# Kernel tuning notes

Measured on AMD Instinct MI355X. Metric: run time of the kernel, lower is better.

Reference implementation:

```python
import jax, jax.numpy as jnp
import numpy as np

POS_TH = 0.5
NEG_TH = 0.4
NEGPOS_RATIO = 3
BBOX_ALPHA = 1.5
CONF_ALPHA = 1.0
VAR_CXCY = 0.1
VAR_WH = 0.2
NUM_CLASSES = 41
B, P, G = 8, 100000, 16


def setup_inputs() -> dict:
    key = jax.random.key(0)
    k = jax.random.split(key, 8)
    loc_data = jax.random.normal(k[0], (B, P, 4), dtype=jnp.float32)
    conf_data = jax.random.normal(k[1], (B, P, NUM_CLASSES), dtype=jnp.float32)
    # priors in (cx, cy, w, h), normalized coords
    p_cxy = jax.random.uniform(k[2], (P, 2), minval=0.0, maxval=1.0)
    p_wh = jax.random.uniform(k[3], (P, 2), minval=0.02, maxval=0.3)
    priors = jnp.concatenate([p_cxy, p_wh], axis=1).astype(jnp.float32)
    # gt boxes in point form (x1, y1, x2, y2)
    g_cxy = jax.random.uniform(k[4], (B, G, 2), minval=0.15, maxval=0.85)
    g_wh = jax.random.uniform(k[5], (B, G, 2), minval=0.05, maxval=0.4)
    gt_boxes = jnp.concatenate([
        jnp.clip(g_cxy - g_wh / 2, 0.0, 1.0),
        jnp.clip(g_cxy + g_wh / 2, 0.0, 1.0),
    ], axis=-1).astype(jnp.float32)
    gt_labels = jax.random.randint(k[6], (B, G), 1, NUM_CLASSES)
    return {"loc_data": loc_data, "conf_data": conf_data, "priors": priors,
            "gt_boxes": gt_boxes, "gt_labels": gt_labels}


def point_form(pr):
    return jnp.concatenate([pr[:, :2] - pr[:, 2:] / 2,
                            pr[:, :2] + pr[:, 2:] / 2], axis=1)


def jaccard(a, b):
    # a: [G,4] xyxy, b: [P,4] xyxy -> [G,P]
    lt = jnp.maximum(a[:, None, :2], b[None, :, :2])
    rb = jnp.minimum(a[:, None, 2:], b[None, :, 2:])
    wh = jnp.clip(rb - lt, 0.0)
    inter = wh[..., 0] * wh[..., 1]
    area_a = ((a[:, 2] - a[:, 0]) * (a[:, 3] - a[:, 1]))[:, None]
    area_b = ((b[:, 2] - b[:, 0]) * (b[:, 3] - b[:, 1]))[None, :]
    return inter / (area_a + area_b - inter)


def encode(matched, priors):
    # matched [P,4] xyxy, priors [P,4] cxcywh -> SSD offsets with variances
    g_cxcy = ((matched[:, :2] + matched[:, 2:]) / 2 - priors[:, :2]) / (VAR_CXCY * priors[:, 2:])
    g_wh = jnp.log(jnp.clip((matched[:, 2:] - matched[:, :2]) / priors[:, 2:], 1e-8)) / VAR_WH
    return jnp.concatenate([g_cxcy, g_wh], axis=1)


def match_one(gt_box, gt_label, priors):
    # gt_box [G,4], gt_label [G], priors [P,4] -> loc_t [P,4], conf_t [P]
    pf = point_form(priors)
    ov = jaccard(gt_box, pf)                      # [G,P]
    best_truth_ov = ov.max(axis=0)                # [P]
    best_truth_idx = ov.argmax(axis=0)            # [P]
    best_prior_idx = ov.argmax(axis=1)            # [G] best prior per gt
    # force-match each gt to its best prior
    best_truth_ov = best_truth_ov.at[best_prior_idx].set(2.0)
    best_truth_idx = best_truth_idx.at[best_prior_idx].set(jnp.arange(gt_box.shape[0]))
    conf = gt_label[best_truth_idx]
    conf = jnp.where(best_truth_ov < POS_TH, -1, conf)   # neutral
    conf = jnp.where(best_truth_ov < NEG_TH, 0, conf)    # background
    loc = encode(gt_box[best_truth_idx], priors)
    return loc, conf


def reference(loc_data, conf_data, priors, gt_boxes, gt_labels):
    bsz, n_pri, n_cls = conf_data.shape
    loc_t, conf_t = jax.vmap(match_one, in_axes=(0, 0, None))(gt_boxes, gt_labels, priors)
    pos = conf_t > 0                               # [B,P]
    num_pos = pos.sum(axis=1)                      # [B]
    # pos_weights: uniform 1/num_pos per image (ones split then normalized)
    pos_w = pos.astype(loc_data.dtype) / jnp.clip(num_pos, 1).astype(loc_data.dtype)[:, None]
    # localization: weighted SmoothL1 over positives
    d = loc_data - loc_t
    sl1 = jnp.where(jnp.abs(d) < 1.0, 0.5 * d * d, jnp.abs(d) - 0.5)
    loss_B = (pos_w[..., None] * sl1).sum() * BBOX_ALPHA
    # OHEM hard negative mining on background-suppression loss
    loss_c = jax.nn.logsumexp(conf_data, axis=-1) - conf_data[..., 0]
    loss_c = jnp.where(pos | (conf_t < 0), 0.0, loss_c)
    order = jnp.argsort(-loss_c, axis=1)
    rank = jnp.argsort(order, axis=1)
    num_neg = jnp.clip(NEGPOS_RATIO * num_pos, 0, n_pri - 1)
    neg = (rank < num_neg[:, None]) & (~pos) & (conf_t >= 0)
    keep = (pos | neg).astype(conf_data.dtype)
    logp = jax.nn.log_softmax(conf_data, axis=-1)
    ce = -jnp.take_along_axis(logp, jnp.clip(conf_t, 0)[..., None], axis=-1)[..., 0]
    total_pos = jnp.clip(num_pos.sum(), 1).astype(conf_data.dtype)
    loss_C = (ce * keep).sum() * CONF_ALPHA / total_pos
    return (loss_B + loss_C) / bsz
```

## Files before the change

kernel.cpp:

```cpp
#include <hip/hip_runtime.h>
#include <stdint.h>

#define BATCH 8
#define NPRI 100000
#define NGT 16
#define NCLS 41
#define F_POS_TH 0.5f
#define F_NEG_TH 0.4f

static constexpr int WTPB = 64;
static constexpr int CPT = WTPB * NCLS / 4;
static constexpr int BLK_PER_B = 224;
static constexpr int TILES_PER_B = (NPRI + WTPB - 1) / WTPB;
static constexpr int H0BIN = 256;
static constexpr int NBIN = 4096;

static constexpr size_t OFF_KEY  = 0;
static constexpr size_t OFF_GTC  = OFF_KEY + (size_t)BATCH*NPRI*4;
static constexpr size_t OFF_HG   = OFF_GTC + BATCH*NGT*8;
static constexpr size_t OFF_NPOS = OFF_HG + (size_t)BATCH*H0BIN*4;
static constexpr size_t OFF_SL1  = OFF_NPOS + BATCH*4;
static constexpr size_t OFF_CEP  = OFF_SL1  + BATCH*4;
static constexpr size_t OFF_NEG  = OFF_CEP  + BATCH*4;
static constexpr size_t OFF_FTK  = OFF_NEG  + BATCH*4;
static constexpr int ZERO_U32 = (int)((OFF_FTK + 4 - OFF_HG) / 4);

typedef float f32x4 __attribute__((ext_vector_type(4)));

__device__ inline float smoothl1(float d) {
  float a = fabsf(d);
  return a < 1.f ? 0.5f * d * d : a - 0.5f;
}
__device__ inline float sl1_terms(f32x4 pv, f32x4 ld, f32x4 gv) {
  float tx = ((gv[0] + gv[2]) * 0.5f - pv[0]) / (0.1f * pv[2]);
  float ty = ((gv[1] + gv[3]) * 0.5f - pv[1]) / (0.1f * pv[3]);
  float tw = __logf(fmaxf((gv[2] - gv[0]) / pv[2], 1e-8f)) / 0.2f;
  float th = __logf(fmaxf((gv[3] - gv[1]) / pv[3], 1e-8f)) / 0.2f;
  return smoothl1(ld[0] - tx) + smoothl1(ld[1] - ty)
       + smoothl1(ld[2] - tw) + smoothl1(ld[3] - th);
}
__device__ inline float aload_f32(const float* p) {
  return __hip_atomic_load(p, __ATOMIC_RELAXED, __HIP_MEMORY_SCOPE_AGENT);
}
__device__ inline unsigned aload_u32(const unsigned* p) {
  return __hip_atomic_load(p, __ATOMIC_RELAXED, __HIP_MEMORY_SCOPE_AGENT);
}
__device__ __forceinline__ void gll16(const void* gsrc, void* ldst) {
  __builtin_amdgcn_global_load_lds(
      (const __attribute__((address_space(1))) void*)gsrc,
      (__attribute__((address_space(3))) void*)ldst, 16, 0, 0);
}

__global__ void k_init(unsigned* __restrict__ z, unsigned long long* __restrict__ gtc) {
  int t = threadIdx.x;
  for (int i = t; i < ZERO_U32; i += 512) z[i] = 0u;
  if (t < BATCH * NGT) gtc[t] = 0xFFFFFFFFull;
}

__global__ __launch_bounds__(WTPB) void k_conf(
    const float* __restrict__ loc, const float* __restrict__ conf,
    const float* __restrict__ priors, const float* __restrict__ gtb,
    const int* __restrict__ gtl,
    unsigned* __restrict__ key, unsigned* __restrict__ histg,
    unsigned long long* __restrict__ gtc,
    unsigned* __restrict__ npos, float* __restrict__ sl1sum, float* __restrict__ cepos) {
  __shared__ float buf[2][CPT * 4];
  __shared__ unsigned hcb[H0BIN];
  __shared__ unsigned long long best[NGT];
  int t = threadIdx.x;
  int b = blockIdx.x / BLK_PER_B;
  int sub = blockIdx.x % BLK_PER_B;
  const f32x4* conf4 = (const f32x4*)conf;
  const size_t bbase4 = (size_t)b * NPRI * NCLS / 4;
  const size_t maxc4 = (size_t)BATCH * NPRI * NCLS / 4 - 1;
  float acc_s = 0.f, acc_c = 0.f; unsigned acc_p = 0;
#pragma unroll
  for (int u = 0; u < H0BIN / WTPB; u++) hcb[t + u * WTPB] = 0u;
  if (t < NGT) best[t] = 0;

  {
    size_t base4 = bbase4 + (size_t)sub * CPT;
#pragma unroll
    for (int u = 0; u < 10; u++) {
      size_t g4 = base4 + (unsigned)(t + u * WTPB);
      if (g4 > maxc4) g4 = maxc4;
      gll16(conf4 + g4, &buf[0][(t + u * WTPB) * 4]);
    }
    if (t < CPT - 10 * WTPB) {
      size_t g4 = base4 + (unsigned)(t + 10 * WTPB);
      if (g4 > maxc4) g4 = maxc4;
      gll16(conf4 + g4, &buf[0][(t + 10 * WTPB) * 4]);
    }
  }
  int cur = 0;
  for (int tidx = sub; tidx < TILES_PER_B; tidx += BLK_PER_B) {
    int p = tidx * WTPB + t;
    bool valid = p < NPRI;
    int pc = valid ? p : NPRI - 1;
    f32x4 pv = ((const f32x4*)priors)[pc];
    f32x4 ld = ((const f32x4*)loc)[(size_t)b * NPRI + pc];
    int nxt = tidx + BLK_PER_B;
    if (nxt < TILES_PER_B) {
      size_t base4 = bbase4 + (size_t)nxt * CPT;
#pragma unroll
      for (int u = 0; u < 10; u++) {
        size_t g4 = base4 + (unsigned)(t + u * WTPB);
        if (g4 > maxc4) g4 = maxc4;
        gll16(conf4 + g4, &buf[cur ^ 1][(t + u * WTPB) * 4]);
      }
      if (t < CPT - 10 * WTPB) {
        size_t g4 = base4 + (unsigned)(t + 10 * WTPB);
        if (g4 > maxc4) g4 = maxc4;
        gll16(conf4 + g4, &buf[cur ^ 1][(t + 10 * WTPB) * 4]);
      }
      asm volatile("s_waitcnt vmcnt(11)" ::: "memory");
    } else {
      asm volatile("s_waitcnt vmcnt(0)" ::: "memory");
    }
    __builtin_amdgcn_sched_barrier(0);
    unsigned kkreg = 0u;
    if (valid) {
      float px1 = pv[0] - 0.5f * pv[2], py1 = pv[1] - 0.5f * pv[3];
      float px2 = pv[0] + 0.5f * pv[2], py2 = pv[1] + 0.5f * pv[3];
      float parea = (px2 - px1) * (py2 - py1);
      float bov = 0.f; int g = 0;
#pragma unroll
      for (int gg = 0; gg < NGT; gg++) {
        const f32x4 gv = ((const f32x4*)gtb)[b * NGT + gg];
        float ix = fmaxf(fminf(px2, gv[2]) - fmaxf(px1, gv[0]), 0.f);
        float iy = fmaxf(fminf(py2, gv[3]) - fmaxf(py1, gv[1]), 0.f);
        float inter = ix * iy;
        float garea = (gv[2] - gv[0]) * (gv[3] - gv[1]);
        float iou = inter / (parea + garea - inter);
        if (iou > bov) { bov = iou; g = gg; }
        if (iou > 0.f) {
          unsigned long long comp = ((unsigned long long)__float_as_uint(iou) << 32)
                                  | (unsigned long long)(0xFFFFFFFFu - (unsigned)p);
          if (comp > best[gg]) atomicMax(&best[gg], comp);
        }
      }
      int c = gtl[b * NGT + g];
      if (bov < F_POS_TH) c = -1;
      if (bov < F_NEG_TH) c = 0;
      const float* r = &buf[cur][t * NCLS];
      float s = 0.f, r0 = 0.f, rc = 0.f;
#pragma unroll
      for (int j = 0; j < NCLS; j++) {
        float v = r[j];
        s += __expf(v);
        if (j == 0) r0 = v;
        if (j == c) rc = v;
      }
      float lse = __logf(s);
      kkreg = (c == 0) ? __float_as_uint(lse - r0) : 0u;
      key[(size_t)b * NPRI + p] = kkreg;
      if (c > 0) {
        acc_p += 1;
        acc_c += lse - rc;
        const f32x4 gvb = ((const f32x4*)gtb)[b * NGT + g];
        acc_s += sl1_terms(pv, ld, gvb);
      }
    }
    unsigned bin = kkreg >> 24;
    unsigned long long m40 = __ballot(valid && kkreg != 0u && bin == 0x40u);
    unsigned long long m00 = __ballot(valid && kkreg == 0u);
    if (m40 && t == __ffsll((long long)m40) - 1)
      atomicAdd(&hcb[0x40], (unsigned)__popcll(m40));
    if (m00 && t == __ffsll((long long)m00) - 1)
      atomicAdd(&hcb[0], (unsigned)__popcll(m00));
    if (valid && kkreg != 0u && bin != 0x40u) atomicAdd(&hcb[bin], 1u);
    cur ^= 1;
  }
  if (t < NGT && best[t] != 0) atomicMax(&gtc[b * NGT + t], best[t]);
#pragma unroll
  for (int u = 0; u < H0BIN / WTPB; u++) {
    unsigned v = hcb[t + u * WTPB];
    if (v) atomicAdd(&histg[b * H0BIN + t + u * WTPB], v);
  }
  float vs = acc_s, vc = acc_c; unsigned vp = acc_p;
#pragma unroll
  for (int off = 32; off; off >>= 1) {
    vs += __shfl_down(vs, off, 64);
    vc += __shfl_down(vc, off, 64);
    vp += __shfl_down(vp, off, 64);
  }
  if (t == 0) {
    if (vp) atomicAdd(&npos[b], vp);
    if (vs != 0.f) atomicAdd(&sl1sum[b], vs);
    if (vc != 0.f) atomicAdd(&cepos[b], vc);
  }
}

__global__ __launch_bounds__(1024) void k_select(
    const float* __restrict__ loc, const float* __restrict__ conf,
    const float* __restrict__ priors, const float* __restrict__ gtb,
    const int* __restrict__ gtl, const unsigned long long* __restrict__ gtc,
    unsigned* __restrict__ key, const unsigned* __restrict__ histg,
    unsigned* __restrict__ npos, float* __restrict__ sl1sum,
    float* __restrict__ cepos, float* __restrict__ negsum,
    unsigned* __restrict__ final_tk, float* __restrict__ out) {
  __shared__ unsigned hc[NBIN];
  __shared__ unsigned h0s[H0BIN];
  __shared__ unsigned pcs[256], sc[256];
  __shared__ int wA; __shared__ unsigned kexA;
  __shared__ unsigned kS, prefS;
  __shared__ float redf[16];
  __shared__ unsigned pw16[NGT]; __shared__ float lse16[NGT], bov16[NGT];
  __shared__ int bidx16[NGT];
  int b = blockIdx.x, t = threadIdx.x;
  if (t < H0BIN) h0s[t] = histg[b * H0BIN + t];
  if (t < NGT) {
    unsigned long long c64 = gtc[b * NGT + t];
    unsigned p = 0xFFFFFFFFu - (unsigned)(c64 & 0xFFFFFFFFull);
    pw16[t] = p;
    const float* row = conf + ((size_t)b * NPRI + p) * NCLS;
    float s = 0.f;
    for (int j = 0; j < NCLS; j++) s += __expf(row[j]);
    lse16[t] = __logf(s);
    f32x4 pv = ((const f32x4*)priors)[p];
    float px1 = pv[0] - 0.5f * pv[2], py1 = pv[1] - 0.5f * pv[3];
    float px2 = pv[0] + 0.5f * pv[2], py2 = pv[1] + 0.5f * pv[3];
    float parea = (px2 - px1) * (py2 - py1);
    float bov = 0.f; int g = 0;
    for (int gg = 0; gg < NGT; gg++) {
      const f32x4 gv = ((const f32x4*)gtb)[b * NGT + gg];
      float ix = fmaxf(fminf(px2, gv[2]) - fmaxf(px1, gv[0]), 0.f);
      float iy = fmaxf(fminf(py2, gv[3]) - fmaxf(py1, gv[1]), 0.f);
      float inter = ix * iy;
      float garea = (gv[2] - gv[0]) * (gv[3] - gv[1]);
      float iou = inter / (parea + garea - inter);
      if (iou > bov) { bov = iou; g = gg; }
    }
    bov16[t] = bov; bidx16[t] = g;
  }
  __syncthreads();
  if (t == 0) {
    unsigned np = npos[b];
    float sl = sl1sum[b], cpv = cepos[b];
    for (int i = 0; i < NGT; i++) {
      unsigned p = pw16[i];
      int prev = -1;
      for (int j = 0; j < i; j++) if (pw16[j] == p) prev = j;
      float lse = lse16[i];
      const float* row = conf + ((size_t)b * NPRI + p) * NCLS;
      f32x4 pv = ((const f32x4*)priors)[p];
      f32x4 ldv = ((const f32x4*)loc)[(size_t)b * NPRI + p];
      float newce = lse - row[gtl[b * NGT + i]];
      float newsl = sl1_terms(pv, ldv, ((const f32x4*)gtb)[b * NGT + i]);
      if (prev < 0) {
        float o = bov16[i]; int gold = bidx16[i];
        int cold = (o < F_NEG_TH) ? 0 : ((o < F_POS_TH) ? -1 : gtl[b * NGT + gold]);
        if (cold == 0) {
          unsigned ko = key[(size_t)b * NPRI + p];
          h0s[ko >> 24] -= 1u; h0s[0] += 1u;
        } else if (cold > 0) {
          np -= 1; cpv -= lse - row[cold];
          sl -= sl1_terms(pv, ldv, ((const f32x4*)gtb)[b * NGT + gold]);
        }
        np += 1; cpv += newce; sl += newsl;
        key[(size_t)b * NPRI + p] = 0u;
      } else {
        cpv -= lse - row[gtl[b * NGT + prev]];
        sl -= sl1_terms(pv, ldv, ((const f32x4*)gtb)[b * NGT + prev]);
        cpv += newce; sl += newsl;
      }
    }
    npos[b] = np; sl1sum[b] = sl; cepos[b] = cpv;
    kS = 0u; prefS = 0u; wA = -1;
  }
  __syncthreads();
  unsigned k0 = min(3u * npos[b], (unsigned)(NPRI - 1));
  const int iters = (NPRI + 1023) / 1024;
  if (t < 256) { unsigned v = h0s[t]; pcs[t] = v; sc[t] = v; }
  __syncthreads();
  for (int off = 1; off < 256; off <<= 1) {
    unsigned v = 0;
    if (t < 256) v = (t + off < 256) ? sc[t + off] : 0u;
    __syncthreads();
    if (t < 256) sc[t] += v;
    __syncthreads();
  }
  if (t < 256) {
    unsigned excl = sc[t] - pcs[t];
    if (k0 > 0 && excl < k0 && k0 <= excl + pcs[t]) { wA = t; kexA = excl; }
  }
  __syncthreads();
  if (t == 0 && wA >= 0) { prefS = ((unsigned)wA) << 24; kS = k0 - kexA; }
  __syncthreads();
  for (int lvl = 1; lvl <= 2; lvl++) {
    unsigned k = kS;
    int shift = (lvl == 1) ? 12 : 0;
    int lowcut = (lvl == 1) ? 24 : 12;
    for (int i = t; i < NBIN; i += 1024) hc[i] = 0u;
    if (t == 0) wA = -1;
    __syncthreads();
    unsigned pre = prefS >> lowcut;
    if (k > 0) {
      for (int n = 0; n < iters; n++) {
        int i = n * 1024 + t;
        if (i < NPRI) {
          unsigned kk = key[(size_t)b * NPRI + i];
          if ((kk >> lowcut) == pre) atomicAdd(&hc[(kk >> shift) & 0xFFFu], 1u);
        }
      }
    }
    __syncthreads();
    if (t < 256) {
      unsigned cs = 0;
#pragma unroll
      for (int u = 0; u < 16; u++) cs += hc[t * 16 + u];
      pcs[t] = cs; sc[t] = cs;
    }
    __syncthreads();
    for (int off = 1; off < 256; off <<= 1) {
      unsigned v = 0;
      if (t < 256) v = (t + off < 256) ? sc[t + off] : 0u;
      __syncthreads();
      if (t < 256) sc[t] += v;
      __syncthreads();
    }
    if (t < 256) {
      unsigned excl = sc[t] - pcs[t];
      if (k > 0 && excl < k && k <= excl + pcs[t]) { wA = t; kexA = excl; }
    }
    __syncthreads();
    if (wA >= 0 && t < 64) {
      int w = wA; unsigned exw = kexA;
      unsigned v = (t < 16) ? hc[w * 16 + t] : 0u;
      unsigned sufv = v;
#pragma unroll
      for (int off = 1; off < 16; off <<= 1) {
        unsigned x = __shfl_down(sufv, off, 64);
        if (t + off < 16) sufv += x;
      }
      unsigned excl2 = exw + (sufv - v);
      if (t < 16 && excl2 < k && k <= excl2 + v) {
        prefS |= ((unsigned)(w * 16 + t)) << shift;
        kS = k - excl2;
      }
    }
    __syncthreads();
  }
  unsigned Tu = prefS;
  unsigned tie = kS;
  float acc = 0.f;
  if (k0 > 0) {
    for (int n = 0; n < iters; n++) {
      int i = n * 1024 + t;
      if (i < NPRI) {
        unsigned kk = key[(size_t)b * NPRI + i];
        if (kk > Tu) acc += __uint_as_float(kk);
      }
    }
  }
#pragma unroll
  for (int off = 32; off; off >>= 1) acc += __shfl_down(acc, off, 64);
  if ((t & 63) == 0) redf[t >> 6] = acc;
  __syncthreads();
  if (t == 0) {
    float tot = 0.f;
    for (int wv = 0; wv < 16; wv++) tot += redf[wv];
    if (k0 > 0) tot += (float)tie * __uint_as_float(Tu);
    negsum[b] = tot;
    __threadfence();
    unsigned r2 = atomicAdd(final_tk, 1u);
    if (r2 == BATCH - 1) {
      __threadfence();
      float lb = 0.f, ctot = 0.f; unsigned tp = 0;
      for (int bb = 0; bb < BATCH; bb++) {
        unsigned nb = aload_u32(&npos[bb]);
        lb += aload_f32(&sl1sum[bb]) / fmaxf((float)nb, 1.f);
        tp += nb;
        ctot += aload_f32(&cepos[bb]) + aload_f32(&negsum[bb]);
      }
      out[0] = (1.5f * lb + ctot / fmaxf((float)tp, 1.f)) / (float)BATCH;
      *final_tk = 0;
    }
  }
}

extern "C" void kernel_launch(void* const* d_in, const int* in_sizes, int n_in,
                              void* d_out, int out_size, void* d_ws, size_t ws_size,
                              hipStream_t stream) {
  const float* loc = (const float*)d_in[0];
  const float* conf = (const float*)d_in[1];
  const float* priors = (const float*)d_in[2];
  const float* gtb = (const float*)d_in[3];
  const int* gtl = (const int*)d_in[4];
  char* ws = (char*)d_ws;
  unsigned* key = (unsigned*)(ws + OFF_KEY);
  unsigned long long* gtc = (unsigned long long*)(ws + OFF_GTC);
  unsigned* histg = (unsigned*)(ws + OFF_HG);
  unsigned* npos = (unsigned*)(ws + OFF_NPOS);
  float* sl1sum = (float*)(ws + OFF_SL1);
  float* cepos = (float*)(ws + OFF_CEP);
  float* negsum = (float*)(ws + OFF_NEG);
  unsigned* final_tk = (unsigned*)(ws + OFF_FTK);
  float* out = (float*)d_out;

  k_init<<<1, 512, 0, stream>>>(histg, gtc);
  k_conf<<<BATCH * BLK_PER_B, WTPB, 0, stream>>>(loc, conf, priors, gtb, gtl,
                                                 key, histg, gtc, npos, sl1sum, cepos);
  k_select<<<BATCH, 1024, 0, stream>>>(loc, conf, priors, gtb, gtl, gtc,
                                       key, histg, npos, sl1sum, cepos,
                                       negsum, final_tk, out);
}
```

Before: 178.2 us.

## Replace LDS-staged persistent conf loop with coalesced register loads and LDS atomic row sums

The persistent 64-thread block that double-buffered conf rows into LDS via global_load_lds is replaced by a one-tile-per-wave grid of 256-thread blocks. Each lane reads coalesced float4 chunks of the tile directly into registers, computes exp values and accumulates per-prior sums with LDS float atomics, and handles rows that straddle a chunk boundary. The class logit for positives is then gathered from global memory. This trades the async LDS copy pipeline for more parallel blocks and register prefetch, at the cost of many LDS atomics and a scattered extra load per positive.

```diff
diff --git a/kernel.cpp b/kernel.cpp
--- a/kernel.cpp
+++ b/kernel.cpp
@@ -8,10 +8,9 @@
 #define F_POS_TH 0.5f
 #define F_NEG_TH 0.4f
 
-static constexpr int WTPB = 64;
-static constexpr int CPT = WTPB * NCLS / 4;
-static constexpr int BLK_PER_B = 224;
-static constexpr int TILES_PER_B = (NPRI + WTPB - 1) / WTPB;
+static constexpr int TILES_PER_B = (NPRI + 63) / 64;
+static constexpr int CBLK = (TILES_PER_B + 3) / 4;
+static constexpr int CW = 64 * NCLS / 4;
 static constexpr int H0BIN = 256;
 static constexpr int NBIN = 4096;
 
@@ -45,11 +44,6 @@
 __device__ inline unsigned aload_u32(const unsigned* p) {
   return __hip_atomic_load(p, __ATOMIC_RELAXED, __HIP_MEMORY_SCOPE_AGENT);
 }
-__device__ __forceinline__ void gll16(const void* gsrc, void* ldst) {
-  __builtin_amdgcn_global_load_lds(
-      (const __attribute__((address_space(1))) void*)gsrc,
-      (__attribute__((address_space(3))) void*)ldst, 16, 0, 0);
-}
 
 __global__ void k_init(unsigned* __restrict__ z, unsigned long long* __restrict__ gtc) {
   int t = threadIdx.x;
@@ -57,67 +51,70 @@
   if (t < BATCH * NGT) gtc[t] = 0xFFFFFFFFull;
 }
 
-__global__ __launch_bounds__(WTPB) void k_conf(
+__global__ __launch_bounds__(256) void k_conf(
     const float* __restrict__ loc, const float* __restrict__ conf,
     const float* __restrict__ priors, const float* __restrict__ gtb,
     const int* __restrict__ gtl,
     unsigned* __restrict__ key, unsigned* __restrict__ histg,
     unsigned long long* __restrict__ gtc,
     unsigned* __restrict__ npos, float* __restrict__ sl1sum, float* __restrict__ cepos) {
-  __shared__ float buf[2][CPT * 4];
+  __shared__ float sums[4][64];
+  __shared__ float r0s[4][64];
   __shared__ unsigned hcb[H0BIN];
   __shared__ unsigned long long best[NGT];
-  int t = threadIdx.x;
-  int b = blockIdx.x / BLK_PER_B;
-  int sub = blockIdx.x % BLK_PER_B;
-  const f32x4* conf4 = (const f32x4*)conf;
-  const size_t bbase4 = (size_t)b * NPRI * NCLS / 4;
-  const size_t maxc4 = (size_t)BATCH * NPRI * NCLS / 4 - 1;
-  float acc_s = 0.f, acc_c = 0.f; unsigned acc_p = 0;
-#pragma unroll
-  for (int u = 0; u < H0BIN / WTPB; u++) hcb[t + u * WTPB] = 0u;
+  __shared__ float redS[4], redC[4]; __shared__ unsigned redP[4];
+  const int t = threadIdx.x, w = t >> 6, l = t & 63;
+  const int b = blockIdx.y;
+  const int tile = blockIdx.x * 4 + w;
+  hcb[t] = 0u;
   if (t < NGT) best[t] = 0;
-
-  {
-    size_t base4 = bbase4 + (size_t)sub * CPT;
-#pragma unroll
-    for (int u = 0; u < 10; u++) {
-      size_t g4 = base4 + (unsigned)(t + u * WTPB);
-      if (g4 > maxc4) g4 = maxc4;
-      gll16(conf4 + g4, &buf[0][(t + u * WTPB) * 4]);
-    }
-    if (t < CPT - 10 * WTPB) {
-      size_t g4 = base4 + (unsigned)(t + 10 * WTPB);
-      if (g4 > maxc4) g4 = maxc4;
-      gll16(conf4 + g4, &buf[0][(t + 10 * WTPB) * 4]);
-    }
-  }
-  int cur = 0;
-  for (int tidx = sub; tidx < TILES_PER_B; tidx += BLK_PER_B) {
-    int p = tidx * WTPB + t;
-    bool valid = p < NPRI;
-    int pc = valid ? p : NPRI - 1;
-    f32x4 pv = ((const f32x4*)priors)[pc];
-    f32x4 ld = ((const f32x4*)loc)[(size_t)b * NPRI + pc];
-    int nxt = tidx + BLK_PER_B;
-    if (nxt < TILES_PER_B) {
-      size_t base4 = bbase4 + (size_t)nxt * CPT;
-#pragma unroll
-      for (int u = 0; u < 10; u++) {
-        size_t g4 = base4 + (unsigned)(t + u * WTPB);
-        if (g4 > maxc4) g4 = maxc4;
-        gll16(conf4 + g4, &buf[cur ^ 1][(t + u * WTPB) * 4]);
-      }
-      if (t < CPT - 10 * WTPB) {
-        size_t g4 = base4 + (unsigned)(t + 10 * WTPB);
-        if (g4 > maxc4) g4 = maxc4;
-        gll16(conf4 + g4, &buf[cur ^ 1][(t + 10 * WTPB) * 4]);
-      }
-      asm volatile("s_waitcnt vmcnt(11)" ::: "memory");
-    } else {
-      asm volatile("s_waitcnt vmcnt(0)" ::: "memory");
-    }
-    __builtin_amdgcn_sched_barrier(0);
+  sums[w][l] = 0.f;
+  __syncthreads();
+  float accS = 0.f, accC = 0.f; unsigned accP = 0;
+  if (tile < TILES_PER_B) {
+    const f32x4* c4b = (const f32x4*)conf + (size_t)b * (NPRI * NCLS / 4);
+    const unsigned bend = (unsigned)(NPRI * NCLS / 4 - 1);
+    const unsigned tbase = (unsigned)tile * CW;
+    const int p = tile * 64 + l;
+    const bool valid = p < NPRI;
+    const int pc = valid ? p : NPRI - 1;
+    const f32x4 pv = ((const f32x4*)priors)[pc];
+    const f32x4 ld = ((const f32x4*)loc)[(size_t)b * NPRI + pc];
+    f32x4 cA = c4b[min(tbase + (unsigned)l, bend)];
+#pragma unroll
+    for (int u = 0; u < 11; u++) {
+      f32x4 cB;
+      {
+        unsigned cn = (unsigned)((u + 1) * 64 + l);
+        cn = cn < (unsigned)CW ? cn : (unsigned)(CW - 1);
+        cB = c4b[min(tbase + cn, bend)];
+      }
+      int cidx = u * 64 + l;
+      if (cidx < CW) {
+        int f = cidx * 4;
+        int r0 = (int)((unsigned)f / 41u);
+        int rem = f - r0 * 41;
+        float e0 = __expf(cA[0]);
+        float e1 = __expf(cA[1]);
+        float e2 = __expf(cA[2]);
+        float e3 = __expf(cA[3]);
+        int nlo = 41 - rem;
+        float slo = e0, shi = 0.f;
+        if (nlo > 1) slo += e1; else shi += e1;
+        if (nlo > 2) slo += e2; else shi += e2;
+        if (nlo > 3) slo += e3; else shi += e3;
+        atomicAdd(&sums[w][r0], slo);
+        if (nlo <= 3) atomicAdd(&sums[w][r0 + 1], shi);
+        if (rem == 0) r0s[w][r0] = cA[0];
+        else if (nlo <= 3) {
+          float v = (nlo == 1) ? cA[1] : (nlo == 2) ? cA[2] : cA[3];
+          r0s[w][r0 + 1] = v;
+        }
+      }
+      cA = cB;
+    }
+    float lse = __logf(sums[w][l]);
+    float r0v = r0s[w][l];
     unsigned kkreg = 0u;
     if (valid) {
       float px1 = pv[0] - 0.5f * pv[2], py1 = pv[1] - 0.5f * pv[3];
@@ -142,52 +139,44 @@
       int c = gtl[b * NGT + g];
       if (bov < F_POS_TH) c = -1;
       if (bov < F_NEG_TH) c = 0;
-      const float* r = &buf[cur][t * NCLS];
-      float s = 0.f, r0 = 0.f, rc = 0.f;
-#pragma unroll
-      for (int j = 0; j < NCLS; j++) {
-        float v = r[j];
-        s += __expf(v);
-        if (j == 0) r0 = v;
-        if (j == c) rc = v;
-      }
-      float lse = __logf(s);
-      kkreg = (c == 0) ? __float_as_uint(lse - r0) : 0u;
+      kkreg = (c == 0) ? __float_as_uint(lse - r0v) : 0u;
       key[(size_t)b * NPRI + p] = kkreg;
       if (c > 0) {
-        acc_p += 1;
-        acc_c += lse - rc;
+        accP = 1;
+        float rc = conf[((size_t)b * NPRI + p) * NCLS + c];
+        accC = lse - rc;
         const f32x4 gvb = ((const f32x4*)gtb)[b * NGT + g];
-        acc_s += sl1_terms(pv, ld, gvb);
+        accS = sl1_terms(pv, ld, gvb);
       }
     }
     unsigned bin = kkreg >> 24;
     unsigned long long m40 = __ballot(valid && kkreg != 0u && bin == 0x40u);
     unsigned long long m00 = __ballot(valid && kkreg == 0u);
-    if (m40 && t == __ffsll((long long)m40) - 1)
+    if (m40 && l == __ffsll((long long)m40) - 1)
       atomicAdd(&hcb[0x40], (unsigned)__popcll(m40));
-    if (m00 && t == __ffsll((long long)m00) - 1)
+    if (m00 && l == __ffsll((long long)m00) - 1)
       atomicAdd(&hcb[0], (unsigned)__popcll(m00));
     if (valid && kkreg != 0u && bin != 0x40u) atomicAdd(&hcb[bin], 1u);
-    cur ^= 1;
-  }
+  }
+  __syncthreads();
   if (t < NGT && best[t] != 0) atomicMax(&gtc[b * NGT + t], best[t]);
-#pragma unroll
-  for (int u = 0; u < H0BIN / WTPB; u++) {
-    unsigned v = hcb[t + u * WTPB];
-    if (v) atomicAdd(&histg[b * H0BIN + t + u * WTPB], v);
-  }
-  float vs = acc_s, vc = acc_c; unsigned vp = acc_p;
+  { unsigned v = hcb[t]; if (v) atomicAdd(&histg[b * H0BIN + t], v); }
+  float vs = accS, vc = accC; unsigned vp = accP;
 #pragma unroll
   for (int off = 32; off; off >>= 1) {
     vs += __shfl_down(vs, off, 64);
     vc += __shfl_down(vc, off, 64);
     vp += __shfl_down(vp, off, 64);
   }
+  if (l == 0) { redS[w] = vs; redC[w] = vc; redP[w] = vp; }
+  __syncthreads();
   if (t == 0) {
-    if (vp) atomicAdd(&npos[b], vp);
-    if (vs != 0.f) atomicAdd(&sl1sum[b], vs);
-    if (vc != 0.f) atomicAdd(&cepos[b], vc);
+    float ts = redS[0] + redS[1] + redS[2] + redS[3];
+    float tc = redC[0] + redC[1] + redC[2] + redC[3];
+    unsigned tp = redP[0] + redP[1] + redP[2] + redP[3];
+    if (tp) atomicAdd(&npos[b], tp);
+    if (ts != 0.f) atomicAdd(&sl1sum[b], ts);
+    if (tc != 0.f) atomicAdd(&cepos[b], tc);
   }
 }
 
@@ -399,8 +388,9 @@
   float* out = (float*)d_out;
 
   k_init<<<1, 512, 0, stream>>>(histg, gtc);
-  k_conf<<<BATCH * BLK_PER_B, WTPB, 0, stream>>>(loc, conf, priors, gtb, gtl,
-                                                 key, histg, gtc, npos, sl1sum, cepos);
+  dim3 gridC(CBLK, BATCH);
+  k_conf<<<gridC, 256, 0, stream>>>(loc, conf, priors, gtb, gtl,
+                                    key, histg, gtc, npos, sl1sum, cepos);
   k_select<<<BATCH, 1024, 0, stream>>>(loc, conf, priors, gtb, gtl, gtc,
                                        key, histg, npos, sl1sum, cepos,
                                        negsum, final_tk, out);
```

Measured after the change: 218.1 us. +22.4%, slower.
